# Kernel tuning notes

Hardware: AMD Instinct MI355X
Metric: run time of the kernel (lower is better)

Reference implementation:

```python
import jax, jax.numpy as jnp
from jax import lax
import numpy as np

CLASS_NUMBER = 19
REGION_RADIUS = 1
KERNEL = 2 * REGION_RADIUS + 1  # 3
IMAGE_TOPK = 256
EPS = 1e-6


def setup_inputs() -> dict:
    key = jax.random.key(0)
    # softmax-like probabilities over classes
    raw = jax.random.uniform(key, (4, CLASS_NUMBER, 512, 1024), dtype=jnp.float32)
    logit = raw / jnp.sum(raw, axis=1, keepdims=True)
    return {"logit": logit}


def _box_sum(x):
    # kxk box sum with zero padding (SAME for odd kernel == pad=radius)
    return lax.reduce_window(x, jnp.float32(0), lax.add,
                             (1, 1, KERNEL, KERNEL), (1, 1, 1, 1), 'SAME')


def reference(logit):
    B, C, H, W = logit.shape
    logC = jnp.log(jnp.float32(C))

    # region uncertainty: normalized entropy, then avg-pool (count_include_pad)
    entropy = jnp.sum(-logit * jnp.log(logit + EPS), axis=1, keepdims=True) / logC
    region_uncertainty = _box_sum(entropy) / (KERNEL * KERNEL)  # [B,1,H,W]

    # region impurity: argmax -> one-hot -> depthwise box-sum (ones kernel)
    predict = jnp.argmax(logit, axis=1)                       # [B,H,W]
    one_hot = jax.nn.one_hot(predict, C, axis=1, dtype=logit.dtype)  # [B,C,H,W]
    summary = _box_sum(one_hot)                               # [B,C,H,W]
    count = jnp.sum(summary, axis=1, keepdims=True)           # [B,1,H,W]
    dist = summary / count
    region_impurity = jnp.sum(-dist * jnp.log(dist + EPS), axis=1, keepdims=True) / logC

    score = region_uncertainty * region_impurity              # [B,1,H,W]

    # per-image score: sum of top-k region scores
    flat = score.reshape(B, H * W)
    topk_vals, _ = lax.top_k(flat, IMAGE_TOPK)
    image_score = jnp.sum(topk_vals, axis=1)                  # [B]
    return image_score
```

## Files before the change

kernel.cpp:

```cpp
#include <hip/hip_runtime.h>
#include <cstdint>
#include <cstddef>

#define BB 4
#define CC 19
#define HH 512
#define WW 1024
#define HW (HH*WW)
#define HW4 (HW/4)
#define BHW (BB*HW)
#define KTOP 256
#define EPSF 1e-6f
#define NB1 8192
#define SEG 128
#define LOGC 2.9444389791664403f

__device__ __forceinline__ unsigned int sortable(float x) {
    unsigned int u = __float_as_uint(x);
    return (u & 0x80000000u) ? ~u : (u | 0x80000000u);
}
__device__ __forceinline__ float unsortable(unsigned int K) {
    unsigned int u = (K & 0x80000000u) ? (K & 0x7FFFFFFFu) : ~K;
    return __uint_as_float(u);
}

__global__ __launch_bounds__(256) void k_ent(const float4* __restrict__ logit,
                                             float4* __restrict__ ent,
                                             uchar4* __restrict__ pred,
                                             unsigned int* __restrict__ histz,
                                             float* __restrict__ outz) {
    int idx = blockIdx.x * 256 + threadIdx.x;
    if (idx < 98312) histz[idx] = 0;
    if (idx < BB) outz[idx] = 0.f;
    int b = idx >> 17;
    int q = idx & (HW4 - 1);
    const float4* base = logit + (size_t)b * CC * HW4 + q;
    float e0 = 0.f, e1 = 0.f, e2 = 0.f, e3 = 0.f;
    float m0 = -1.f, m1 = -1.f, m2 = -1.f, m3 = -1.f;
    int a0 = 0, a1 = 0, a2 = 0, a3 = 0;
#pragma unroll
    for (int c = 0; c < CC; ++c) {
        float4 p = base[(size_t)c * HW4];
        e0 -= p.x * __logf(p.x + EPSF); if (p.x > m0) { m0 = p.x; a0 = c; }
        e1 -= p.y * __logf(p.y + EPSF); if (p.y > m1) { m1 = p.y; a1 = c; }
        e2 -= p.z * __logf(p.z + EPSF); if (p.z > m2) { m2 = p.z; a2 = c; }
        e3 -= p.w * __logf(p.w + EPSF); if (p.w > m3) { m3 = p.w; a3 = c; }
    }
    ent[idx] = make_float4(e0, e1, e2, e3);
    pred[idx] = make_uchar4((unsigned char)a0, (unsigned char)a1,
                            (unsigned char)a2, (unsigned char)a3);
}

__global__ __launch_bounds__(256) void k_score_hist(const float* __restrict__ ent,
                                                    const unsigned char* __restrict__ pred,
                                                    float* __restrict__ score,
                                                    unsigned int* __restrict__ hist1) {
    __shared__ unsigned int lh[NB1];
    int b = blockIdx.x >> 7;
    int seg = blockIdx.x & (SEG - 1);
    for (int i = threadIdx.x; i < NB1; i += 256) lh[i] = 0;
    __syncthreads();
    const float* eb = ent + (size_t)b * HW;
    const unsigned char* pb = pred + (size_t)b * HW;
    int base = seg * (HW / SEG);

    for (int it = 0; it < 16; ++it) {
        int hw = base + it * 256 + threadIdx.x;
        int h = hw >> 10;
        int w = hw & (WW - 1);

        float es = 0.f;
        int cls[9];
        int nv = 0;
#pragma unroll
        for (int i = 0; i < 9; ++i) {
            int dh = i / 3 - 1, dw = i % 3 - 1;
            int hh = h + dh, ww = w + dw;
            bool ok = (hh >= 0) & (hh < HH) & (ww >= 0) & (ww < WW);
            int o = ok ? ((hh << 10) | ww) : 0;
            es += ok ? eb[o] : 0.f;
            cls[i] = ok ? (int)pb[o] : 255;
            nv += ok ? 1 : 0;
        }
        float inv = 1.f / (float)nv;
        float lsum = 0.f;
#pragma unroll
        for (int i = 0; i < 9; ++i) {
            int cnt = 0;
#pragma unroll
            for (int j = 0; j < 9; ++j) cnt += (cls[j] == cls[i]) ? 1 : 0;
            float lg = __logf((float)cnt * inv + EPSF);
            lsum += (cls[i] != 255) ? lg : 0.f;
        }
        float imp = -inv * lsum;
        float v = (es * (1.f / (9.f * LOGC))) * (imp * (1.f / LOGC));
        score[(size_t)b * HW + hw] = v;
        atomicAdd(&lh[sortable(v) >> 19], 1u);
    }
    __syncthreads();
    unsigned int* hb = hist1 + (size_t)b * NB1;
    for (int i = threadIdx.x; i < NB1; i += 256) {
        unsigned int c = lh[i];
        if (c) atomicAdd(&hb[i], c);
    }
}

__device__ __forceinline__ void select_bin(const unsigned int* __restrict__ hb,
                                           int rem, int* bin_out, int* rem_out) {
    __shared__ unsigned int cs[256];
    __shared__ unsigned int bs[32];
    __shared__ int s_chunk, s_bin, s_rem;
    int t = threadIdx.x;
    unsigned int s = 0;
#pragma unroll 8
    for (int i = 0; i < 32; ++i) s += hb[t * 32 + i];
    cs[t] = s;
    __syncthreads();
    for (int d = 1; d < 256; d <<= 1) {
        unsigned int v = (t + d < 256) ? cs[t + d] : 0;
        __syncthreads();
        cs[t] += v;
        __syncthreads();
    }
    unsigned int St = cs[t];
    unsigned int St1 = (t < 255) ? cs[t + 1] : 0;
    if ((int)St >= rem && (t == 255 || (int)St1 < rem)) {
        s_chunk = t;
        s_rem = rem - (int)St1;
    }
    __syncthreads();
    int chunk = s_chunk;
    int rem2 = s_rem;
    if (t < 32) bs[t] = hb[chunk * 32 + t];
    __syncthreads();
    for (int d = 1; d < 32; d <<= 1) {
        unsigned int v = (t < 32 && t + d < 32) ? bs[t + d] : 0;
        __syncthreads();
        if (t < 32) bs[t] += v;
        __syncthreads();
    }
    if (t < 32) {
        unsigned int Sb = bs[t];
        unsigned int Sb1 = (t < 31) ? bs[t + 1] : 0;
        if ((int)Sb >= rem2 && (t == 31 || (int)Sb1 < rem2)) {
            s_bin = chunk * 32 + t;
            s_rem = rem2 - (int)Sb1;
        }
    }
    __syncthreads();
    *bin_out = s_bin;
    *rem_out = s_rem;
}

__global__ __launch_bounds__(256) void k_scan1(const unsigned int* __restrict__ hist1,
                                               unsigned int* __restrict__ T1,
                                               int* __restrict__ r1) {
    int b = blockIdx.x;
    int bin, rem;
    select_bin(hist1 + (size_t)b * NB1, KTOP, &bin, &rem);
    if (threadIdx.x == 0) { T1[b] = (unsigned int)bin; r1[b] = rem; }
}

__global__ __launch_bounds__(256) void k_hist2(const float4* __restrict__ score,
                                               const unsigned int* __restrict__ T1,
                                               unsigned int* __restrict__ hist2,
                                               float* __restrict__ hsum,
                                               float* __restrict__ out) {
    __shared__ unsigned int lh[NB1];
    __shared__ float ls[NB1];
    __shared__ float red[4];
    int b = blockIdx.x >> 7;
    int seg = blockIdx.x & (SEG - 1);
    for (int i = threadIdx.x; i < NB1; i += 256) { lh[i] = 0; ls[i] = 0.f; }
    __syncthreads();
    unsigned int t1 = T1[b];
    const float4* p = score + ((size_t)b * HW + (size_t)seg * (HW / SEG)) / 4;
    float sa = 0.f;
    for (int i = threadIdx.x; i < (HW / SEG) / 4; i += 256) {
        float4 v = p[i];
        float vv[4] = {v.x, v.y, v.z, v.w};
#pragma unroll
        for (int q = 0; q < 4; ++q) {
            unsigned int k = sortable(vv[q]);
            unsigned int cb = k >> 19;
            if (cb > t1) sa += vv[q];
            else if (cb == t1) {
                int sub = (k >> 6) & 0x1FFF;
                atomicAdd(&lh[sub], 1u);
                atomicAdd(&ls[sub], vv[q]);
            }
        }
    }
    __syncthreads();
    unsigned int* hb = hist2 + (size_t)b * NB1;
    float* sb = hsum + (size_t)b * NB1;
    for (int i = threadIdx.x; i < NB1; i += 256) {
        unsigned int c = lh[i];
        if (c) { atomicAdd(&hb[i], c); atomicAdd(&sb[i], ls[i]); }
    }
#pragma unroll
    for (int d = 32; d; d >>= 1) sa += __shfl_down(sa, d);
    if ((threadIdx.x & 63) == 0) red[threadIdx.x >> 6] = sa;
    __syncthreads();
    if (threadIdx.x == 0) {
        float tt = red[0] + red[1] + red[2] + red[3];
        if (tt != 0.f) atomicAdd(&out[b], tt);
    }
}

__global__ __launch_bounds__(256) void k_scan2(const unsigned int* __restrict__ hist2,
                                               const float* __restrict__ hsum,
                                               const unsigned int* __restrict__ T1,
                                               const int* __restrict__ r1,
                                               float* __restrict__ out) {
    int b = blockIdx.x;
    int bin, rem;
    select_bin(hist2 + (size_t)b * NB1, r1[b], &bin, &rem);
    __shared__ float rs[256];
    int t = threadIdx.x;
    const float* sb = hsum + (size_t)b * NB1;
    float s = 0.f;
    for (int i = t; i < NB1; i += 256) if (i > bin) s += sb[i];
    rs[t] = s;
    __syncthreads();
    for (int d = 128; d; d >>= 1) {
        if (t < d) rs[t] += rs[t + d];
        __syncthreads();
    }
    if (t == 0) {
        unsigned int K = (T1[b] << 19) | ((unsigned int)bin << 6);
        out[b] += rs[0] + unsortable(K) * (float)rem;
    }
}

extern "C" void kernel_launch(void* const* d_in, const int* in_sizes, int n_in,
                              void* d_out, int out_size, void* d_ws, size_t ws_size,
                              hipStream_t stream) {
    const float* logit = (const float*)d_in[0];
    float* out = (float*)d_out;
    char* ws = (char*)d_ws;

    float*         ent   = (float*)(ws);
    unsigned char* pred  = (unsigned char*)(ws + 8388608);
    float*         score = (float*)(ws + 10485760);
    unsigned int*  histb = (unsigned int*)(ws + 18874368);
    unsigned int*  hist1 = histb;
    unsigned int*  hist2 = histb + 32768;
    float*         hsum  = (float*)(histb + 65536);
    unsigned int*  T1    = histb + 98304;
    int*           r1    = (int*)(histb + 98308);

    k_ent<<<BHW / 4 / 256, 256, 0, stream>>>((const float4*)logit, (float4*)ent,
                                             (uchar4*)pred, histb, out);
    k_score_hist<<<BB * SEG, 256, 0, stream>>>(ent, pred, score, hist1);
    k_scan1<<<BB, 256, 0, stream>>>(hist1, T1, r1);
    k_hist2<<<BB * SEG, 256, 0, stream>>>((const float4*)score, T1, hist2, hsum, out);
    k_scan2<<<BB, 256, 0, stream>>>(hist2, hsum, T1, r1, out);
}
```

Measured before the change: 298.3 us.

## Fuse entropy/argmax and score computation into one tiled kernel with halo

Replaces the separate entropy/argmax pass and score/histogram pass with a single kernel that loads a 34x34 halo tile of the logits, computes entropy and argmax into shared memory, then computes the 3x3 region scores and the local histogram. This drops the global round trip of the entropy and prediction maps and one kernel launch. In exchange each block recomputes halo pixels (about 13% extra logit reads), loses float4 vectorized loads, and uses more shared memory per block, which may limit occupancy. Zeroing of the histogram and output buffers moves to hipMemsetAsync calls.

```diff
diff --git a/kernel.cpp b/kernel.cpp
--- a/kernel.cpp
+++ b/kernel.cpp
@@ -7,12 +7,13 @@
 #define HH 512
 #define WW 1024
 #define HW (HH*WW)
-#define HW4 (HW/4)
 #define BHW (BB*HW)
 #define KTOP 256
 #define EPSF 1e-6f
 #define NB1 8192
 #define SEG 128
+#define TS 32
+#define THALO 34
 #define LOGC 2.9444389791664403f
 
 __device__ __forceinline__ unsigned int sortable(float x) {
@@ -24,64 +25,59 @@
     return __uint_as_float(u);
 }
 
-__global__ __launch_bounds__(256) void k_ent(const float4* __restrict__ logit,
-                                             float4* __restrict__ ent,
-                                             uchar4* __restrict__ pred,
-                                             unsigned int* __restrict__ histz,
-                                             float* __restrict__ outz) {
-    int idx = blockIdx.x * 256 + threadIdx.x;
-    if (idx < 98312) histz[idx] = 0;
-    if (idx < BB) outz[idx] = 0.f;
-    int b = idx >> 17;
-    int q = idx & (HW4 - 1);
-    const float4* base = logit + (size_t)b * CC * HW4 + q;
-    float e0 = 0.f, e1 = 0.f, e2 = 0.f, e3 = 0.f;
-    float m0 = -1.f, m1 = -1.f, m2 = -1.f, m3 = -1.f;
-    int a0 = 0, a1 = 0, a2 = 0, a3 = 0;
-#pragma unroll
-    for (int c = 0; c < CC; ++c) {
-        float4 p = base[(size_t)c * HW4];
-        e0 -= p.x * __logf(p.x + EPSF); if (p.x > m0) { m0 = p.x; a0 = c; }
-        e1 -= p.y * __logf(p.y + EPSF); if (p.y > m1) { m1 = p.y; a1 = c; }
-        e2 -= p.z * __logf(p.z + EPSF); if (p.z > m2) { m2 = p.z; a2 = c; }
-        e3 -= p.w * __logf(p.w + EPSF); if (p.w > m3) { m3 = p.w; a3 = c; }
-    }
-    ent[idx] = make_float4(e0, e1, e2, e3);
-    pred[idx] = make_uchar4((unsigned char)a0, (unsigned char)a1,
-                            (unsigned char)a2, (unsigned char)a3);
-}
-
-__global__ __launch_bounds__(256) void k_score_hist(const float* __restrict__ ent,
-                                                    const unsigned char* __restrict__ pred,
-                                                    float* __restrict__ score,
-                                                    unsigned int* __restrict__ hist1) {
+__global__ __launch_bounds__(256) void k_fused(const float* __restrict__ logit,
+                                               float* __restrict__ score,
+                                               unsigned int* __restrict__ hist1) {
+    __shared__ float ent[THALO * THALO];
+    __shared__ int prd[THALO * THALO];
     __shared__ unsigned int lh[NB1];
-    int b = blockIdx.x >> 7;
-    int seg = blockIdx.x & (SEG - 1);
+    int blk = blockIdx.x;
+    int b = blk >> 9;
+    int tile = blk & 511;
+    int ty = tile >> 5, tx = tile & 31;
+    int h0 = ty * TS, w0 = tx * TS;
+
     for (int i = threadIdx.x; i < NB1; i += 256) lh[i] = 0;
-    __syncthreads();
-    const float* eb = ent + (size_t)b * HW;
-    const unsigned char* pb = pred + (size_t)b * HW;
-    int base = seg * (HW / SEG);
-
-    for (int it = 0; it < 16; ++it) {
-        int hw = base + it * 256 + threadIdx.x;
-        int h = hw >> 10;
-        int w = hw & (WW - 1);
-
+
+    for (int k = 0; k < 5; ++k) {
+        int p = threadIdx.x + k * 256;
+        if (p < THALO * THALO) {
+            int ly = p / THALO, lx = p - ly * THALO;
+            int gy = h0 - 1 + ly, gx = w0 - 1 + lx;
+            bool ok = (gy >= 0) & (gy < HH) & (gx >= 0) & (gx < WW);
+            float e = 0.f; float m = -1.f; int am = 255;
+            if (ok) {
+                const float* base = logit + (size_t)b * CC * HW + gy * WW + gx;
+                am = 0;
+#pragma unroll
+                for (int c = 0; c < CC; ++c) {
+                    float pv = base[(size_t)c * HW];
+                    e -= pv * __logf(pv + EPSF);
+                    if (pv > m) { m = pv; am = c; }
+                }
+            }
+            ent[p] = e;
+            prd[p] = am;
+        }
+    }
+    __syncthreads();
+
+    float* sbuf = score + (size_t)b * HW;
+#pragma unroll
+    for (int q = 0; q < 4; ++q) {
+        int pix = threadIdx.x + q * 256;
+        int py = pix >> 5, px = pix & 31;
+        int h = h0 + py, w = w0 + px;
+        int lbase = py * THALO + px;
         float es = 0.f;
         int cls[9];
-        int nv = 0;
 #pragma unroll
         for (int i = 0; i < 9; ++i) {
-            int dh = i / 3 - 1, dw = i % 3 - 1;
-            int hh = h + dh, ww = w + dw;
-            bool ok = (hh >= 0) & (hh < HH) & (ww >= 0) & (ww < WW);
-            int o = ok ? ((hh << 10) | ww) : 0;
-            es += ok ? eb[o] : 0.f;
-            cls[i] = ok ? (int)pb[o] : 255;
-            nv += ok ? 1 : 0;
-        }
+            int o = lbase + (i / 3) * THALO + (i % 3);
+            es += ent[o];
+            cls[i] = prd[o];
+        }
+        int nv = ((h > 0) + (h < HH - 1) + 1) * ((w > 0) + (w < WW - 1) + 1);
         float inv = 1.f / (float)nv;
         float lsum = 0.f;
 #pragma unroll
@@ -94,7 +90,7 @@
         }
         float imp = -inv * lsum;
         float v = (es * (1.f / (9.f * LOGC))) * (imp * (1.f / LOGC));
-        score[(size_t)b * HW + hw] = v;
+        sbuf[h * WW + w] = v;
         atomicAdd(&lh[sortable(v) >> 19], 1u);
     }
     __syncthreads();
@@ -240,19 +236,18 @@
     float* out = (float*)d_out;
     char* ws = (char*)d_ws;
 
-    float*         ent   = (float*)(ws);
-    unsigned char* pred  = (unsigned char*)(ws + 8388608);
-    float*         score = (float*)(ws + 10485760);
-    unsigned int*  histb = (unsigned int*)(ws + 18874368);
+    float*         score = (float*)(ws);
+    unsigned int*  histb = (unsigned int*)(ws + 8388608);
     unsigned int*  hist1 = histb;
     unsigned int*  hist2 = histb + 32768;
     float*         hsum  = (float*)(histb + 65536);
     unsigned int*  T1    = histb + 98304;
     int*           r1    = (int*)(histb + 98308);
 
-    k_ent<<<BHW / 4 / 256, 256, 0, stream>>>((const float4*)logit, (float4*)ent,
-                                             (uchar4*)pred, histb, out);
-    k_score_hist<<<BB * SEG, 256, 0, stream>>>(ent, pred, score, hist1);
+    hipMemsetAsync(histb, 0, 393248, stream);
+    hipMemsetAsync(d_out, 0, (size_t)out_size * sizeof(float), stream);
+
+    k_fused<<<BB * 512, 256, 0, stream>>>(logit, score, hist1);
     k_scan1<<<BB, 256, 0, stream>>>(hist1, T1, r1);
     k_hist2<<<BB * SEG, 256, 0, stream>>>((const float4*)score, T1, hist2, hsum, out);
     k_scan2<<<BB, 256, 0, stream>>>(hist2, hsum, T1, r1, out);
```

New measurement: 305.2 us. 2.3% more time.
